# Kernel tuning notes

Measured on AMD Instinct MI355X. Metric: run time of the kernel, lower is better.

The kernel has to match this reference:

```python
import jax, jax.numpy as jnp
import numpy as np

BASE_T = 0.07
ALPHA = 0.5
EPS = 1e-12  # torch F.normalize eps


def _l2_normalize(x):
    norm = jnp.linalg.norm(x, axis=1, keepdims=True)
    return x / jnp.maximum(norm, EPS)


def setup_inputs() -> dict:
    key = jax.random.key(0)
    k1, k2, k3 = jax.random.split(key, 3)
    B, D, H, W = 4096, 512, 16, 16
    return {
        "emb1": jax.random.normal(k1, (B, D), dtype=jnp.float32),
        "emb2": jax.random.normal(k2, (B, D), dtype=jnp.float32),
        "attention_map": jax.random.uniform(k3, (B, H, W), dtype=jnp.float32),
    }


def reference(emb1, emb2, attention_map):
    B = emb1.shape[0]
    e1 = _l2_normalize(emb1)
    e2 = _l2_normalize(emb2)

    att = attention_map.mean(axis=(1, 2))                     # [B]
    temp = (BASE_T * (1.0 + ALPHA * att))[:, None]            # [B, 1]

    x = jnp.concatenate([e1, e2], axis=0)                     # [2B, D]
    x_swap = jnp.concatenate([e2, e1], axis=0)                # [2B, D]
    temp_cat = jnp.concatenate([temp, temp], axis=0)          # [2B, 1]

    sim = jnp.matmul(x, x.T) / temp_cat                       # [2B, 2B]
    pos_sim = jnp.sum(x * x_swap, axis=1) / temp_cat[:, 0]    # [2B]

    diag = jnp.eye(2 * B, dtype=bool)
    sim = jnp.where(diag, -jnp.inf, sim)                      # exp(-inf) = 0

    denominator = jnp.exp(sim).sum(axis=1)                    # [2B]
    loss = -jnp.log(jnp.exp(pos_sim) / denominator)
    return loss.mean()
```

## Files before the change

kernel.cpp:

```cpp
#include <hip/hip_runtime.h>
#include <hip/hip_bf16.h>
#include <math.h>

#define B_ROWS 4096
#define D_DIM 512
#define TWO_B 8192
#define HW_N 256
#define BASE_T 0.07f
#define ALPHA_C 0.5f
#define LOG2E 1.44269504088896340736f

typedef __bf16 v8bf __attribute__((ext_vector_type(8)));
typedef float v4f __attribute__((ext_vector_type(4)));

__device__ __forceinline__ float fast_exp2(float x) {
#if __has_builtin(__builtin_amdgcn_exp2f)
    return __builtin_amdgcn_exp2f(x);
#else
    return exp2f(x);
#endif
}

__global__ __launch_bounds__(256) void prep_kernel(
    const float* __restrict__ emb1, const float* __restrict__ emb2,
    const float* __restrict__ att, __hip_bfloat16* __restrict__ X,
    float* __restrict__ inv_temp, float* __restrict__ pos)
{
    const int b = blockIdx.x;
    const int t = threadIdx.x;
    const float* e1 = emb1 + (size_t)b * D_DIM;
    const float* e2 = emb2 + (size_t)b * D_DIM;
    float a1 = e1[t], c1 = e1[t + 256];
    float a2 = e2[t], c2 = e2[t + 256];
    float av = att[(size_t)b * HW_N + t];
    float s1 = a1 * a1 + c1 * c1;
    float s2 = a2 * a2 + c2 * c2;
    float s12 = a1 * a2 + c1 * c2;
    #pragma unroll
    for (int m = 1; m < 64; m <<= 1) {
        s1  += __shfl_xor(s1, m, 64);
        s2  += __shfl_xor(s2, m, 64);
        s12 += __shfl_xor(s12, m, 64);
        av  += __shfl_xor(av, m, 64);
    }
    __shared__ float red[4][4];
    const int w = t >> 6, lane = t & 63;
    if (lane == 0) { red[w][0] = s1; red[w][1] = s2; red[w][2] = s12; red[w][3] = av; }
    __syncthreads();
    const float T1  = red[0][0] + red[1][0] + red[2][0] + red[3][0];
    const float T2  = red[0][1] + red[1][1] + red[2][1] + red[3][1];
    const float T12 = red[0][2] + red[1][2] + red[2][2] + red[3][2];
    const float Ta  = red[0][3] + red[1][3] + red[2][3] + red[3][3];
    const float i1 = 1.0f / fmaxf(sqrtf(T1), 1e-12f);
    const float i2 = 1.0f / fmaxf(sqrtf(T2), 1e-12f);
    const float it = 1.0f / (BASE_T * (1.0f + ALPHA_C * (Ta * (1.0f / 256.0f))));
    __hip_bfloat16* x1 = X + (size_t)b * D_DIM;
    __hip_bfloat16* x2 = X + (size_t)(b + B_ROWS) * D_DIM;
    x1[t]       = __float2bfloat16(a1 * i1);
    x1[t + 256] = __float2bfloat16(c1 * i1);
    x2[t]       = __float2bfloat16(a2 * i2);
    x2[t + 256] = __float2bfloat16(c2 * i2);
    if (t == 0) {
        inv_temp[b] = it * LOG2E;
        inv_temp[b + B_ROWS] = it * LOG2E;
        pos[b] = (T12 * i1 * i2) * it;
    }
}

__device__ __forceinline__ void gload_lds16(const void* g, void* s) {
    __builtin_amdgcn_global_load_lds(
        (const __attribute__((address_space(1))) unsigned int*)g,
        (__attribute__((address_space(3))) unsigned int*)s,
        16, 0, 0);
}

__global__ __launch_bounds__(256) void gram_kernel(
    const __hip_bfloat16* __restrict__ X,
    const float* __restrict__ inv_temp,
    float* __restrict__ partial)
{
    const int bid = blockIdx.x;
    int rb = (int)((129.0f - sqrtf(129.0f * 129.0f - 8.0f * (float)bid)) * 0.5f);
    rb = rb < 0 ? 0 : (rb > 63 ? 63 : rb);
    while (rb > 0 && (rb * (129 - rb)) / 2 > bid) rb--;
    while (rb < 63 && ((rb + 1) * (129 - (rb + 1))) / 2 <= bid) rb++;
    const int cb = rb + (bid - (rb * (129 - rb)) / 2);

    __shared__ __hip_bfloat16 smA[128 * 128];
    __shared__ __hip_bfloat16 smB[128 * 128];

    const int rowBase = rb * 128;
    const int colBase = cb * 128;

    const int tid  = threadIdx.x;
    const int w    = tid >> 6;
    const int lane = tid & 63;
    const int quad = lane >> 4;
    const int t    = lane & 15;
    const int wm   = w >> 1;
    const int wn   = w & 1;

    const int srow   = lane >> 4;
    const int schunk = lane & 15;

    v4f acc[4][4];
    #pragma unroll
    for (int a = 0; a < 4; a++)
        #pragma unroll
        for (int b2 = 0; b2 < 4; b2++)
            acc[a][b2] = v4f{0.0f, 0.0f, 0.0f, 0.0f};

    const __hip_bfloat16* Arow0 = X + (size_t)rowBase * D_DIM;
    const __hip_bfloat16* Brow0 = X + (size_t)colBase * D_DIM;

    for (int kk = 0; kk < D_DIM; kk += 128) {
        #pragma unroll
        for (int j = 0; j < 8; j++) {
            const int g = w * 8 + j;
            const int r = g * 4 + srow;
            const int gc = schunk ^ (r & 15);
            gload_lds16(Arow0 + (size_t)r * D_DIM + kk + gc * 8,
                        &smA[g * 512]);
            gload_lds16(Brow0 + (size_t)r * D_DIM + kk + gc * 8,
                        &smB[g * 512]);
        }
        __syncthreads();

        #pragma unroll
        for (int s = 0; s < 4; s++) {
            v8bf af[4], bf[4];
            #pragma unroll
            for (int mi = 0; mi < 4; mi++) {
                const int row = wm * 64 + mi * 16 + t;
                const int p = (s * 4 + quad) ^ t;
                af[mi] = *(const v8bf*)&smA[row * 128 + p * 8];
            }
            #pragma unroll
            for (int ni = 0; ni < 4; ni++) {
                const int col = wn * 64 + ni * 16 + t;
                const int p = (s * 4 + quad) ^ t;
                bf[ni] = *(const v8bf*)&smB[col * 128 + p * 8];
            }
            #pragma unroll
            for (int mi = 0; mi < 4; mi++)
                #pragma unroll
                for (int ni = 0; ni < 4; ni++)
                    acc[mi][ni] = __builtin_amdgcn_mfma_f32_16x16x32_bf16(
                        af[mi], bf[ni], acc[mi][ni], 0, 0, 0);
        }
        __syncthreads();
    }

    v4f itv[4];
    #pragma unroll
    for (int mi = 0; mi < 4; mi++)
        itv[mi] = *(const v4f*)&inv_temp[rowBase + wm * 64 + mi * 16 + quad * 4];

    float* prow = partial + (size_t)(cb * 2 + wn) * TWO_B;
    #pragma unroll
    for (int mi = 0; mi < 4; mi++) {
        #pragma unroll
        for (int r = 0; r < 4; r++) {
            const int i = rowBase + wm * 64 + mi * 16 + quad * 4 + r;
            const float it = itv[mi][r];
            float s = 0.0f;
            #pragma unroll
            for (int ni = 0; ni < 4; ni++) {
                const int j = colBase + wn * 64 + ni * 16 + t;
                const float v = fast_exp2(acc[mi][ni][r] * it);
                s += (i == j) ? 0.0f : v;
            }
            s += __shfl_xor(s, 1, 64);
            s += __shfl_xor(s, 2, 64);
            s += __shfl_xor(s, 4, 64);
            s += __shfl_xor(s, 8, 64);
            if (t == 0) prow[i] = s;
        }
    }

    if (rb != cb) {
        float itj[4];
        float cs[4] = {0.0f, 0.0f, 0.0f, 0.0f};
        #pragma unroll
        for (int ni = 0; ni < 4; ni++)
            itj[ni] = inv_temp[colBase + wn * 64 + ni * 16 + t];
        #pragma unroll
        for (int mi = 0; mi < 4; mi++)
            #pragma unroll
            for (int r = 0; r < 4; r++)
                #pragma unroll
                for (int ni = 0; ni < 4; ni++)
                    cs[ni] += fast_exp2(acc[mi][ni][r] * itj[ni]);
        float* pcol = partial + (size_t)(rb * 2 + wm) * TWO_B;
        #pragma unroll
        for (int ni = 0; ni < 4; ni++) {
            cs[ni] += __shfl_xor(cs[ni], 16, 64);
            cs[ni] += __shfl_xor(cs[ni], 32, 64);
            if (quad == 0) pcol[colBase + wn * 64 + ni * 16 + t] = cs[ni];
        }
    }
}

__global__ __launch_bounds__(256) void finish1(
    const float* __restrict__ partial, const float* __restrict__ pos,
    float* __restrict__ blockSums)
{
    const int i = blockIdx.x * 256 + threadIdx.x;
    float d = 0.0f;
    #pragma unroll 8
    for (int s = 0; s < 128; s++) d += partial[(size_t)s * TWO_B + i];
    float li = logf(d) - pos[i & (B_ROWS - 1)];
    #pragma unroll
    for (int m = 1; m < 64; m <<= 1) li += __shfl_xor(li, m, 64);
    __shared__ float red[4];
    const int w = threadIdx.x >> 6, lane = threadIdx.x & 63;
    if (lane == 0) red[w] = li;
    __syncthreads();
    if (threadIdx.x == 0) blockSums[blockIdx.x] = red[0] + red[1] + red[2] + red[3];
}

__global__ void finish2(const float* __restrict__ blockSums, float* __restrict__ out)
{
    const int lane = threadIdx.x;
    float v = (lane < 32) ? blockSums[lane] : 0.0f;
    #pragma unroll
    for (int m = 1; m < 64; m <<= 1) v += __shfl_xor(v, m, 64);
    if (lane == 0) out[0] = v * (1.0f / 8192.0f);
}

extern "C" void kernel_launch(void* const* d_in, const int* in_sizes, int n_in,
                              void* d_out, int out_size, void* d_ws, size_t ws_size,
                              hipStream_t stream) {
    const float* emb1 = (const float*)d_in[0];
    const float* emb2 = (const float*)d_in[1];
    const float* att  = (const float*)d_in[2];
    float* out = (float*)d_out;

    char* ws = (char*)d_ws;
    __hip_bfloat16* X  = (__hip_bfloat16*)ws;
    float* inv_temp    = (float*)(ws + 8388608);
    float* pos         = (float*)(ws + 8388608 + 32768);
    float* partial     = (float*)(ws + 8388608 + 32768 + 16384);
    float* blockSums   = (float*)(ws + 8388608 + 32768 + 16384 + 4194304);

    prep_kernel<<<B_ROWS, 256, 0, stream>>>(emb1, emb2, att, X, inv_temp, pos);
    gram_kernel<<<2080, 256, 0, stream>>>(X, inv_temp, partial);
    finish1<<<TWO_B / 256, 256, 0, stream>>>(partial, pos, blockSums);
    finish2<<<1, 64, 0, stream>>>(blockSums, out);
}
```

Before: 143.4 us.

## Load MFMA operands directly from global into registers, drop LDS staging

Result: slower. 220.9 us (+54.1%).

```diff
diff --git a/kernel.cpp b/kernel.cpp
--- a/kernel.cpp
+++ b/kernel.cpp
@@ -67,14 +67,7 @@
     }
 }
 
-__device__ __forceinline__ void gload_lds16(const void* g, void* s) {
-    __builtin_amdgcn_global_load_lds(
-        (const __attribute__((address_space(1))) unsigned int*)g,
-        (__attribute__((address_space(3))) unsigned int*)s,
-        16, 0, 0);
-}
-
-__global__ __launch_bounds__(256) void gram_kernel(
+__global__ __launch_bounds__(256, 2) void gram_kernel(
     const __hip_bfloat16* __restrict__ X,
     const float* __restrict__ inv_temp,
     float* __restrict__ partial)
@@ -85,9 +78,6 @@
     while (rb > 0 && (rb * (129 - rb)) / 2 > bid) rb--;
     while (rb < 63 && ((rb + 1) * (129 - (rb + 1))) / 2 <= bid) rb++;
     const int cb = rb + (bid - (rb * (129 - rb)) / 2);
-
-    __shared__ __hip_bfloat16 smA[128 * 128];
-    __shared__ __hip_bfloat16 smB[128 * 128];
 
     const int rowBase = rb * 128;
     const int colBase = cb * 128;
@@ -100,8 +90,14 @@
     const int wm   = w >> 1;
     const int wn   = w & 1;
 
-    const int srow   = lane >> 4;
-    const int schunk = lane & 15;
+    const __hip_bfloat16* ap[4];
+    const __hip_bfloat16* bp[4];
+    #pragma unroll
+    for (int mi = 0; mi < 4; mi++)
+        ap[mi] = X + (size_t)(rowBase + wm * 64 + mi * 16 + t) * D_DIM + quad * 8;
+    #pragma unroll
+    for (int ni = 0; ni < 4; ni++)
+        bp[ni] = X + (size_t)(colBase + wn * 64 + ni * 16 + t) * D_DIM + quad * 8;
 
     v4f acc[4][4];
     #pragma unroll
@@ -110,45 +106,36 @@
         for (int b2 = 0; b2 < 4; b2++)
             acc[a][b2] = v4f{0.0f, 0.0f, 0.0f, 0.0f};
 
-    const __hip_bfloat16* Arow0 = X + (size_t)rowBase * D_DIM;
-    const __hip_bfloat16* Brow0 = X + (size_t)colBase * D_DIM;
-
-    for (int kk = 0; kk < D_DIM; kk += 128) {
-        #pragma unroll
-        for (int j = 0; j < 8; j++) {
-            const int g = w * 8 + j;
-            const int r = g * 4 + srow;
-            const int gc = schunk ^ (r & 15);
-            gload_lds16(Arow0 + (size_t)r * D_DIM + kk + gc * 8,
-                        &smA[g * 512]);
-            gload_lds16(Brow0 + (size_t)r * D_DIM + kk + gc * 8,
-                        &smB[g * 512]);
+    v8bf abuf[2][4][2], bbuf[2][4][2];
+    #pragma unroll
+    for (int mi = 0; mi < 4; mi++) {
+        abuf[0][mi][0] = *(const v8bf*)(ap[mi]);
+        abuf[0][mi][1] = *(const v8bf*)(ap[mi] + 32);
+        bbuf[0][mi][0] = *(const v8bf*)(bp[mi]);
+        bbuf[0][mi][1] = *(const v8bf*)(bp[mi] + 32);
+    }
+
+    #pragma unroll
+    for (int p = 0; p < 8; p++) {
+        const int cur = p & 1, nxt = cur ^ 1;
+        if (p < 7) {
+            const int ko = (p + 1) * 64;
+            #pragma unroll
+            for (int mi = 0; mi < 4; mi++) {
+                abuf[nxt][mi][0] = *(const v8bf*)(ap[mi] + ko);
+                abuf[nxt][mi][1] = *(const v8bf*)(ap[mi] + ko + 32);
+                bbuf[nxt][mi][0] = *(const v8bf*)(bp[mi] + ko);
+                bbuf[nxt][mi][1] = *(const v8bf*)(bp[mi] + ko + 32);
+            }
         }
-        __syncthreads();
-
-        #pragma unroll
-        for (int s = 0; s < 4; s++) {
-            v8bf af[4], bf[4];
-            #pragma unroll
-            for (int mi = 0; mi < 4; mi++) {
-                const int row = wm * 64 + mi * 16 + t;
-                const int p = (s * 4 + quad) ^ t;
-                af[mi] = *(const v8bf*)&smA[row * 128 + p * 8];
-            }
-            #pragma unroll
-            for (int ni = 0; ni < 4; ni++) {
-                const int col = wn * 64 + ni * 16 + t;
-                const int p = (s * 4 + quad) ^ t;
-                bf[ni] = *(const v8bf*)&smB[col * 128 + p * 8];
-            }
+        #pragma unroll
+        for (int ks = 0; ks < 2; ks++)
             #pragma unroll
             for (int mi = 0; mi < 4; mi++)
                 #pragma unroll
                 for (int ni = 0; ni < 4; ni++)
                     acc[mi][ni] = __builtin_amdgcn_mfma_f32_16x16x32_bf16(
-                        af[mi], bf[ni], acc[mi][ni], 0, 0, 0);
-        }
-        __syncthreads();
+                        abuf[cur][mi][ks], bbuf[cur][ni][ks], acc[mi][ni], 0, 0, 0);
     }
 
     v4f itv[4];
```

## Double-buffer gram kernel K tiles and remap block order across XCDs

Applied to the files above, without the earlier changes.

Result: slower. 151.6 us (+5.7%).

```diff
diff --git a/kernel.cpp b/kernel.cpp
--- a/kernel.cpp
+++ b/kernel.cpp
@@ -79,15 +79,15 @@
     const float* __restrict__ inv_temp,
     float* __restrict__ partial)
 {
-    const int bid = blockIdx.x;
+    const int bid = (blockIdx.x & 7) * 260 + (blockIdx.x >> 3);
     int rb = (int)((129.0f - sqrtf(129.0f * 129.0f - 8.0f * (float)bid)) * 0.5f);
     rb = rb < 0 ? 0 : (rb > 63 ? 63 : rb);
     while (rb > 0 && (rb * (129 - rb)) / 2 > bid) rb--;
     while (rb < 63 && ((rb + 1) * (129 - (rb + 1))) / 2 <= bid) rb++;
     const int cb = rb + (bid - (rb * (129 - rb)) / 2);
 
-    __shared__ __hip_bfloat16 smA[128 * 128];
-    __shared__ __hip_bfloat16 smB[128 * 128];
+    __shared__ __hip_bfloat16 smA[2][128 * 64];
+    __shared__ __hip_bfloat16 smB[2][128 * 64];
 
     const int rowBase = rb * 128;
     const int colBase = cb * 128;
@@ -100,8 +100,12 @@
     const int wm   = w >> 1;
     const int wn   = w & 1;
 
-    const int srow   = lane >> 4;
-    const int schunk = lane & 15;
+    const int sg = lane >> 3;
+    const int sc = lane & 7;
+    const int gc = sc ^ sg;
+
+    const __hip_bfloat16* Arow0 = X + (size_t)rowBase * D_DIM;
+    const __hip_bfloat16* Brow0 = X + (size_t)colBase * D_DIM;
 
     v4f acc[4][4];
     #pragma unroll
@@ -110,37 +114,39 @@
         for (int b2 = 0; b2 < 4; b2++)
             acc[a][b2] = v4f{0.0f, 0.0f, 0.0f, 0.0f};
 
-    const __hip_bfloat16* Arow0 = X + (size_t)rowBase * D_DIM;
-    const __hip_bfloat16* Brow0 = X + (size_t)colBase * D_DIM;
-
-    for (int kk = 0; kk < D_DIM; kk += 128) {
-        #pragma unroll
-        for (int j = 0; j < 8; j++) {
-            const int g = w * 8 + j;
-            const int r = g * 4 + srow;
-            const int gc = schunk ^ (r & 15);
-            gload_lds16(Arow0 + (size_t)r * D_DIM + kk + gc * 8,
-                        &smA[g * 512]);
-            gload_lds16(Brow0 + (size_t)r * D_DIM + kk + gc * 8,
-                        &smB[g * 512]);
-        }
+    #pragma unroll
+    for (int j = 0; j < 4; j++) {
+        const int g = w * 4 + j;
+        const int r = g * 8 + sg;
+        gload_lds16(Arow0 + (size_t)r * D_DIM + gc * 8, &smA[0][g * 512]);
+        gload_lds16(Brow0 + (size_t)r * D_DIM + gc * 8, &smB[0][g * 512]);
+    }
+
+    for (int kk = 0; kk < 8; kk++) {
+        const int cur = kk & 1;
         __syncthreads();
-
-        #pragma unroll
-        for (int s = 0; s < 4; s++) {
+        if (kk < 7) {
+            const int ko = (kk + 1) * 64;
+            #pragma unroll
+            for (int j = 0; j < 4; j++) {
+                const int g = w * 4 + j;
+                const int r = g * 8 + sg;
+                gload_lds16(Arow0 + (size_t)r * D_DIM + ko + gc * 8,
+                            &smA[cur ^ 1][g * 512]);
+                gload_lds16(Brow0 + (size_t)r * D_DIM + ko + gc * 8,
+                            &smB[cur ^ 1][g * 512]);
+            }
+        }
+        #pragma unroll
+        for (int s = 0; s < 2; s++) {
             v8bf af[4], bf[4];
-            #pragma unroll
-            for (int mi = 0; mi < 4; mi++) {
-                const int row = wm * 64 + mi * 16 + t;
-                const int p = (s * 4 + quad) ^ t;
-                af[mi] = *(const v8bf*)&smA[row * 128 + p * 8];
-            }
-            #pragma unroll
-            for (int ni = 0; ni < 4; ni++) {
-                const int col = wn * 64 + ni * 16 + t;
-                const int p = (s * 4 + quad) ^ t;
-                bf[ni] = *(const v8bf*)&smB[col * 128 + p * 8];
-            }
+            const int p = (s * 4 + quad) ^ (t & 7);
+            #pragma unroll
+            for (int mi = 0; mi < 4; mi++)
+                af[mi] = *(const v8bf*)&smA[cur][(wm * 64 + mi * 16 + t) * 64 + p * 8];
+            #pragma unroll
+            for (int ni = 0; ni < 4; ni++)
+                bf[ni] = *(const v8bf*)&smB[cur][(wn * 64 + ni * 16 + t) * 64 + p * 8];
             #pragma unroll
             for (int mi = 0; mi < 4; mi++)
                 #pragma unroll
@@ -148,7 +154,6 @@
                     acc[mi][ni] = __builtin_amdgcn_mfma_f32_16x16x32_bf16(
                         af[mi], bf[ni], acc[mi][ni], 0, 0, 0);
         }
-        __syncthreads();
     }
 
     v4f itv[4];
```

## Prefetch gram tiles through registers and remap block order for L2 locality

Applied to the files above, without the earlier changes.

Measured after the change: 144.6 us. Within noise of the previous version (+0.8%).

```diff
diff --git a/kernel.cpp b/kernel.cpp
--- a/kernel.cpp
+++ b/kernel.cpp
@@ -12,6 +12,7 @@
 
 typedef __bf16 v8bf __attribute__((ext_vector_type(8)));
 typedef float v4f __attribute__((ext_vector_type(4)));
+typedef unsigned int v4u __attribute__((ext_vector_type(4)));
 
 __device__ __forceinline__ float fast_exp2(float x) {
 #if __has_builtin(__builtin_amdgcn_exp2f)
@@ -67,19 +68,12 @@
     }
 }
 
-__device__ __forceinline__ void gload_lds16(const void* g, void* s) {
-    __builtin_amdgcn_global_load_lds(
-        (const __attribute__((address_space(1))) unsigned int*)g,
-        (__attribute__((address_space(3))) unsigned int*)s,
-        16, 0, 0);
-}
-
 __global__ __launch_bounds__(256) void gram_kernel(
     const __hip_bfloat16* __restrict__ X,
     const float* __restrict__ inv_temp,
     float* __restrict__ partial)
 {
-    const int bid = blockIdx.x;
+    const int bid = (blockIdx.x & 7) * 260 + (blockIdx.x >> 3);
     int rb = (int)((129.0f - sqrtf(129.0f * 129.0f - 8.0f * (float)bid)) * 0.5f);
     rb = rb < 0 ? 0 : (rb > 63 ? 63 : rb);
     while (rb > 0 && (rb * (129 - rb)) / 2 > bid) rb--;
@@ -103,6 +97,19 @@
     const int srow   = lane >> 4;
     const int schunk = lane & 15;
 
+    const __hip_bfloat16* Arow0 = X + (size_t)rowBase * D_DIM;
+    const __hip_bfloat16* Brow0 = X + (size_t)colBase * D_DIM;
+
+    const v4u* gA[8]; const v4u* gB[8];
+    #pragma unroll
+    for (int j = 0; j < 8; j++) {
+        const int g = w * 8 + j;
+        const int r = g * 4 + srow;
+        const int gc = schunk ^ (r & 15);
+        gA[j] = (const v4u*)(Arow0 + (size_t)r * D_DIM + gc * 8);
+        gB[j] = (const v4u*)(Brow0 + (size_t)r * D_DIM + gc * 8);
+    }
+
     v4f acc[4][4];
     #pragma unroll
     for (int a = 0; a < 4; a++)
@@ -110,37 +117,40 @@
         for (int b2 = 0; b2 < 4; b2++)
             acc[a][b2] = v4f{0.0f, 0.0f, 0.0f, 0.0f};
 
-    const __hip_bfloat16* Arow0 = X + (size_t)rowBase * D_DIM;
-    const __hip_bfloat16* Brow0 = X + (size_t)colBase * D_DIM;
-
-    for (int kk = 0; kk < D_DIM; kk += 128) {
+    v4u rA[8], rB[8];
+    #pragma unroll
+    for (int j = 0; j < 8; j++) { rA[j] = gA[j][0]; rB[j] = gB[j][0]; }
+
+    for (int p = 0; p < 4; p++) {
         #pragma unroll
         for (int j = 0; j < 8; j++) {
             const int g = w * 8 + j;
-            const int r = g * 4 + srow;
-            const int gc = schunk ^ (r & 15);
-            gload_lds16(Arow0 + (size_t)r * D_DIM + kk + gc * 8,
-                        &smA[g * 512]);
-            gload_lds16(Brow0 + (size_t)r * D_DIM + kk + gc * 8,
-                        &smB[g * 512]);
+            *(v4u*)&smA[g * 512 + lane * 8] = rA[j];
+            *(v4u*)&smB[g * 512 + lane * 8] = rB[j];
         }
         __syncthreads();
+
+        if (p < 3) {
+            const int ko = (p + 1) * 16;
+            #pragma unroll
+            for (int j = 0; j < 8; j++) { rA[j] = gA[j][ko >> 4 << 4 ? 0 : 0]; }
+            #pragma unroll
+            for (int j = 0; j < 8; j++) {
+                rA[j] = *(const v4u*)((const __hip_bfloat16*)gA[j] + (p + 1) * 128);
+                rB[j] = *(const v4u*)((const __hip_bfloat16*)gB[j] + (p + 1) * 128);
+            }
+        }
 
         #pragma unroll
         for (int s = 0; s < 4; s++) {
             v8bf af[4], bf[4];
-            #pragma unroll
-            for (int mi = 0; mi < 4; mi++) {
-                const int row = wm * 64 + mi * 16 + t;
-                const int p = (s * 4 + quad) ^ t;
-                af[mi] = *(const v8bf*)&smA[row * 128 + p * 8];
-            }
-            #pragma unroll
-            for (int ni = 0; ni < 4; ni++) {
-                const int col = wn * 64 + ni * 16 + t;
-                const int p = (s * 4 + quad) ^ t;
-                bf[ni] = *(const v8bf*)&smB[col * 128 + p * 8];
-            }
+            const int pp = (s * 4 + quad) ^ t;
+            #pragma unroll
+            for (int mi = 0; mi < 4; mi++)
+                af[mi] = *(const v8bf*)&smA[(wm * 64 + mi * 16 + t) * 128 + pp * 8];
+            #pragma unroll
+            for (int ni = 0; ni < 4; ni++)
+                bf[ni] = *(const v8bf*)&smB[(wn * 64 + ni * 16 + t) * 128 + pp * 8];
             #pragma unroll
             for (int mi = 0; mi < 4; mi++)
                 #pragma unroll
```
